# Performance work log

Hardware: AMD Instinct MI355X
Metric: run time of the kernel (lower is better)

The kernel has to match this reference:

```python
import jax, jax.numpy as jnp
import numpy as np

D_MODEL = 256
INPUT_DIM = 63
NUM_CLASSES = 13
NUM_LAYERS = 4
D_STATE = 128
D_CONV = 4
D_INNER = 512          # expand * d_model
HEADDIM = 64
NHEADS = D_INNER // HEADDIM  # 8
NGROUPS = 1
CONV_DIM = D_INNER + 2 * NGROUPS * D_STATE   # 768
D_IN_PROJ = 2 * D_INNER + 2 * NGROUPS * D_STATE + NHEADS  # 1160
BATCH, SEQLEN = 8, 2048


def setup_inputs() -> dict:
    key = jax.random.key(0)
    ks = jax.random.split(key, 12)
    s = 0.02
    f32 = jnp.float32
    # dt_bias init as in mamba2: inverse-softplus of dt in [1e-3, 1e-1]
    dt = jnp.exp(jax.random.uniform(ks[6], (NUM_LAYERS, NHEADS), f32) * (np.log(0.1) - np.log(0.001)) + np.log(0.001))
    dt_bias = dt + jnp.log(-jnp.expm1(-dt))
    A_log = jnp.log(jax.random.uniform(ks[7], (NUM_LAYERS, NHEADS), f32, 1.0, 16.0))
    return {
        "x": jax.random.normal(ks[0], (BATCH, SEQLEN, INPUT_DIM), f32),
        "in_w": jax.random.normal(ks[1], (D_MODEL, INPUT_DIM), f32) * s,
        "in_b": jnp.zeros((D_MODEL,), f32),
        "ln_in_g": jnp.ones((D_MODEL,), f32),
        "ln_in_b": jnp.zeros((D_MODEL,), f32),
        "inproj_w": jax.random.normal(ks[2], (NUM_LAYERS, D_IN_PROJ, D_MODEL), f32) * s,
        "conv_w": jax.random.normal(ks[3], (NUM_LAYERS, CONV_DIM, D_CONV), f32) * 0.2,
        "conv_b": jnp.zeros((NUM_LAYERS, CONV_DIM), f32),
        "dt_bias": dt_bias,
        "A_log": A_log,
        "D": jnp.ones((NUM_LAYERS, NHEADS), f32),
        "norm_w": jnp.ones((NUM_LAYERS, D_INNER), f32),
        "outproj_w": jax.random.normal(ks[4], (NUM_LAYERS, D_MODEL, D_INNER), f32) * s,
        "ln_g": jnp.ones((NUM_LAYERS, D_MODEL), f32),
        "ln_b": jnp.zeros((NUM_LAYERS, D_MODEL), f32),
        "out_w": jax.random.normal(ks[5], (NUM_CLASSES, D_MODEL), f32) * s,
        "out_b": jnp.zeros((NUM_CLASSES,), f32),
    }


def layernorm(x, g, b, eps=1e-5):
    m = jnp.mean(x, -1, keepdims=True)
    v = jnp.mean(jnp.square(x - m), -1, keepdims=True)
    return (x - m) * jax.lax.rsqrt(v + eps) * g + b


def mamba2_block(x, w_in, cw, cb, dtb, Alog, Dp, nw, w_out):
    # x: (b, l, d_model)
    b, l, _ = x.shape
    zxbcdt = jnp.einsum('bld,ed->ble', x, w_in)                 # (b,l,1160)
    z = zxbcdt[..., :D_INNER]                                   # (b,l,512)
    xBC = zxbcdt[..., D_INNER:D_INNER + CONV_DIM]               # (b,l,768)
    dt = jax.nn.softplus(zxbcdt[..., D_INNER + CONV_DIM:] + dtb)  # (b,l,8)
    # causal depthwise conv1d + silu
    xp = jnp.pad(xBC, ((0, 0), (D_CONV - 1, 0), (0, 0)))
    kern = cw.T[:, None, :]                                     # (K,1,C)
    xBC = jax.lax.conv_general_dilated(
        xp, kern, (1,), 'VALID',
        dimension_numbers=('NWC', 'WIO', 'NWC'),
        feature_group_count=CONV_DIM)
    xBC = jax.nn.silu(xBC + cb)
    xin = xBC[..., :D_INNER].reshape(b, l, NHEADS, HEADDIM)     # (b,l,h,p)
    Bm = xBC[..., D_INNER:D_INNER + D_STATE]                    # (b,l,n)
    Cm = xBC[..., D_INNER + D_STATE:]                           # (b,l,n)
    A = -jnp.exp(Alog)                                          # (h,)
    dA = jnp.exp(dt * A)                                        # (b,l,h)
    dtx = dt[..., None] * xin                                   # (b,l,h,p)

    def step(state, inp):
        dA_t, dtx_t, B_t, C_t = inp                             # (b,h),(b,h,p),(b,n),(b,n)
        state = state * dA_t[..., None, None] + dtx_t[..., None] * B_t[:, None, None, :]
        y_t = jnp.einsum('bhpn,bn->bhp', state, C_t)
        return state, y_t

    state0 = jnp.zeros((b, NHEADS, HEADDIM, D_STATE), x.dtype)
    _, ys = jax.lax.scan(step, state0, (
        dA.transpose(1, 0, 2), dtx.transpose(1, 0, 2, 3),
        Bm.transpose(1, 0, 2), Cm.transpose(1, 0, 2)))
    y = ys.transpose(1, 0, 2, 3) + Dp[:, None] * xin            # (b,l,h,p)
    y = y.reshape(b, l, D_INNER)
    # gated RMSNorm (norm_before_gate=False): rmsnorm(y * silu(z)) * w
    y = y * jax.nn.silu(z)
    y = y * jax.lax.rsqrt(jnp.mean(jnp.square(y), -1, keepdims=True) + 1e-5) * nw
    return jnp.einsum('ble,de->bld', y, w_out)


def reference(x, in_w, in_b, ln_in_g, ln_in_b, inproj_w, conv_w, conv_b,
              dt_bias, A_log, D, norm_w, outproj_w, ln_g, ln_b, out_w, out_b):
    # input projection (dropout is identity in eval mode)
    h = layernorm(jnp.einsum('bli,di->bld', x, in_w) + in_b, ln_in_g, ln_in_b)
    for i in range(NUM_LAYERS):
        res = h
        h = mamba2_block(h, inproj_w[i], conv_w[i], conv_b[i], dt_bias[i],
                         A_log[i], D[i], norm_w[i], outproj_w[i])
        h = layernorm(h + res, ln_g[i], ln_b[i])
    logits = jnp.einsum('bld,cd->blc', h, out_w) + out_b
    return logits.transpose(1, 0, 2)  # (T, N, C) for CTC
```

## Files before the change

### kernel.cpp

```cpp
#include <hip/hip_runtime.h>
#include <math.h>


#define NTOK   16384
#define DMODEL 256
#define DINNER 512
#define DSTATE 128
#define NHEADS 8
#define HEADDIM 64
#define CONVDIM 768
#define DINPROJ 1288
#define NPADIN 1408
#define Q      128
#define NCHUNK 16
#define NBC    128

typedef __attribute__((ext_vector_type(8))) short bf16x8v;
typedef __attribute__((ext_vector_type(4))) float f32x4;
typedef __attribute__((ext_vector_type(8))) unsigned short ush8;
typedef __attribute__((ext_vector_type(4))) unsigned short ush4;

__device__ __forceinline__ float siluf_(float x){ return x / (1.f + expf(-x)); }

__device__ __forceinline__ unsigned short f2bf(float x){
  union { float f; unsigned u; } v; v.f = x;
  unsigned r = v.u + 0x7FFF + ((v.u >> 16) & 1);
  return (unsigned short)(r >> 16);
}
__device__ __forceinline__ float bf2f(unsigned short u){
  union { unsigned u; float f; } v; v.u = ((unsigned)u) << 16; return v.f;
}
__device__ __forceinline__ void g2lds16(const void* g, void* l){
  __builtin_amdgcn_global_load_lds(
      (const __attribute__((address_space(1))) unsigned int*)g,
      (__attribute__((address_space(3))) unsigned int*)l, 16, 0, 0);
}

__global__ __launch_bounds__(256) void k_cast_all(const float* __restrict__ x,
    const float* __restrict__ in_w, const float* __restrict__ inproj_w,
    const float* __restrict__ outproj_w, unsigned short* __restrict__ xb,
    unsigned short* __restrict__ wxb, unsigned short* __restrict__ wbin,
    unsigned short* __restrict__ wbout){
  int idx = blockIdx.x*256 + threadIdx.x;
  if (idx < 1048576){
    int col = idx & 63, row = idx >> 6;
    xb[idx] = (col < 63) ? f2bf(x[(size_t)row*63 + col]) : 0;
    return;
  }
  idx -= 1048576;
  if (idx < 16384){
    int k = idx & 63, n = idx >> 6;
    wxb[idx] = (k < 63) ? f2bf(in_w[(size_t)n*63 + k]) : 0;
    return;
  }
  idx -= 16384;
  if (idx < 1441792){
    int k = idx & 255;
    int n = (idx >> 8) % NPADIN;
    int l = idx / (256*NPADIN);
    wbin[idx] = (n < DINPROJ) ? f2bf(inproj_w[((size_t)l*DINPROJ + n)*256 + k]) : 0;
    return;
  }
  idx -= 1441792;
  if (idx < 524288) wbout[idx] = f2bf(outproj_w[idx]);
}

__global__ __launch_bounds__(256) void gemm_ln(const unsigned short* __restrict__ A,
    const unsigned short* __restrict__ W, float* __restrict__ h,
    unsigned short* __restrict__ hb, const float* __restrict__ g,
    const float* __restrict__ be, int K, int addres){
  __shared__ unsigned short As[64*64];
  __shared__ unsigned short Ws[256*64];
  __shared__ float redS[4][64], redS2[4][64];
  int m0 = blockIdx.x * 64;
  int t = threadIdx.x;
  int wave = t >> 6, lane = t & 63;
  int lr = lane & 15, lk = lane >> 4;
  f32x4 acc[4][4] = {};
  for (int k0=0; k0<K; k0+=64){
    #pragma unroll
    for (int i=0;i<2;i++){
      int seg = i*256 + t;
      int row = seg >> 3, c8 = (seg&7)*8;
      g2lds16(A + (size_t)(m0+row)*K + k0 + c8, (char*)As + seg*16);
    }
    #pragma unroll
    for (int i=0;i<8;i++){
      int seg = i*256 + t;
      int row = seg >> 3, c8 = (seg&7)*8;
      g2lds16(W + (size_t)row*K + k0 + c8, (char*)Ws + seg*16);
    }
    __syncthreads();
    #pragma unroll
    for (int kk=0;kk<2;kk++){
      bf16x8v wf[4], af[4];
      #pragma unroll
      for (int ci=0;ci<4;ci++)
        wf[ci] = *(const bf16x8v*)&Ws[(wave*64 + ci*16 + lr)*64 + kk*32 + lk*8];
      #pragma unroll
      for (int ti=0;ti<4;ti++)
        af[ti] = *(const bf16x8v*)&As[(ti*16 + lr)*64 + kk*32 + lk*8];
      #pragma unroll
      for (int ci=0;ci<4;ci++)
        #pragma unroll
        for (int ti=0;ti<4;ti++)
          acc[ci][ti] = __builtin_amdgcn_mfma_f32_16x16x32_bf16(wf[ci], af[ti], acc[ci][ti],0,0,0);
    }
    __syncthreads();
  }
  float pS[4] = {}, pS2[4] = {};
  #pragma unroll
  for (int ci=0;ci<4;ci++){
    int col = wave*64 + ci*16 + lk*4;
    #pragma unroll
    for (int ti=0;ti<4;ti++){
      int token = m0 + ti*16 + lr;
      if (addres){
        float4 r4 = *(const float4*)&h[(size_t)token*256 + col];
        acc[ci][ti][0]+=r4.x; acc[ci][ti][1]+=r4.y; acc[ci][ti][2]+=r4.z; acc[ci][ti][3]+=r4.w;
      }
      #pragma unroll
      for (int j=0;j<4;j++){ float v = acc[ci][ti][j]; pS[ti]+=v; pS2[ti]+=v*v; }
    }
  }
  #pragma unroll
  for (int ti=0;ti<4;ti++){
    pS[ti]  += __shfl_xor(pS[ti],16);  pS[ti]  += __shfl_xor(pS[ti],32);
    pS2[ti] += __shfl_xor(pS2[ti],16); pS2[ti] += __shfl_xor(pS2[ti],32);
  }
  if (lk == 0){
    #pragma unroll
    for (int ti=0;ti<4;ti++){ redS[wave][ti*16+lr] = pS[ti]; redS2[wave][ti*16+lr] = pS2[ti]; }
  }
  __syncthreads();
  #pragma unroll
  for (int ti=0;ti<4;ti++){
    int rloc = ti*16 + lr;
    float S  = redS[0][rloc]+redS[1][rloc]+redS[2][rloc]+redS[3][rloc];
    float S2 = redS2[0][rloc]+redS2[1][rloc]+redS2[2][rloc]+redS2[3][rloc];
    float mean = S*(1.f/256.f);
    float var  = S2*(1.f/256.f) - mean*mean;
    float r = rsqrtf(var + 1e-5f);
    int token = m0 + rloc;
    #pragma unroll
    for (int ci=0;ci<4;ci++){
      int col = wave*64 + ci*16 + lk*4;
      float o[4];
      #pragma unroll
      for (int j=0;j<4;j++) o[j] = (acc[ci][ti][j]-mean)*r*g[col+j] + be[col+j];
      *(float4*)&h[(size_t)token*256 + col] = make_float4(o[0],o[1],o[2],o[3]);
      ush4 ub = {f2bf(o[0]),f2bf(o[1]),f2bf(o[2]),f2bf(o[3])};
      *(ush4*)&hb[(size_t)token*256 + col] = ub;
    }
  }
}

__global__ __launch_bounds__(256) void gemm_gln(
    const unsigned short* __restrict__ yssmb,
    const unsigned short* __restrict__ zxb,
    const float* __restrict__ nw, const unsigned short* __restrict__ W,
    float* __restrict__ h, unsigned short* __restrict__ hb,
    const float* __restrict__ g, const float* __restrict__ be){
  __shared__ unsigned short As[32*64];
  __shared__ unsigned short Ws[256*64];
  __shared__ float rnS[32];
  __shared__ float redS[4][32], redS2[4][32];
  int m0 = blockIdx.x * 32;
  int t = threadIdx.x;
  int wave = t >> 6, lane = t & 63;
  int lr = lane & 15, lk = lane >> 4;
  int grow = t >> 3;
  int gk   = (t & 7) * 8;
  int gtoken = m0 + grow;
  float s2 = 0.f;
  f32x4 acc[4][2] = {};
  for (int k0=0; k0<512; k0+=64){
    #pragma unroll
    for (int i=0;i<8;i++){
      int sg = i*256 + t;
      int rw = sg >> 3, c8 = (sg&7)*8;
      g2lds16(W + (size_t)rw*DINNER + k0 + c8, (char*)Ws + sg*16);
    }
    {
      int k = k0 + gk;
      ush8 ys = *(const ush8*)&yssmb[(size_t)gtoken*DINNER + k];
      ush8 z8 = *(const ush8*)&zxb[(size_t)gtoken*DINPROJ + k];
      float4 w0 = *(const float4*)&nw[k];
      float4 w1 = *(const float4*)&nw[k+4];
      float nwv[8] = {w0.x,w0.y,w0.z,w0.w,w1.x,w1.y,w1.z,w1.w};
      unsigned short vb[8];
      #pragma unroll
      for (int j=0;j<8;j++){
        float v = bf2f(ys[j]) * siluf_(bf2f(z8[j]));
        s2 += v*v;
        vb[j] = f2bf(v * nwv[j]);
      }
      *(ush8*)&As[grow*64 + gk] = *(ush8*)vb;
    }
    __syncthreads();
    #pragma unroll
    for (int kk=0;kk<2;kk++){
      bf16x8v wf[4], af[2];
      #pragma unroll
      for (int ci=0;ci<4;ci++)
        wf[ci] = *(const bf16x8v*)&Ws[(wave*64 + ci*16 + lr)*64 + kk*32 + lk*8];
      #pragma unroll
      for (int ti=0;ti<2;ti++)
        af[ti] = *(const bf16x8v*)&As[(ti*16 + lr)*64 + kk*32 + lk*8];
      #pragma unroll
      for (int ci=0;ci<4;ci++)
        #pragma unroll
        for (int ti=0;ti<2;ti++)
          acc[ci][ti] = __builtin_amdgcn_mfma_f32_16x16x32_bf16(wf[ci], af[ti], acc[ci][ti],0,0,0);
    }
    __syncthreads();
  }
  s2 += __shfl_xor(s2,1); s2 += __shfl_xor(s2,2); s2 += __shfl_xor(s2,4);
  if ((t & 7) == 0) rnS[grow] = rsqrtf(s2*(1.f/512.f) + 1e-5f);
  __syncthreads();
  float pS[2] = {}, pS2[2] = {};
  #pragma unroll
  for (int ci=0;ci<4;ci++){
    int col = wave*64 + ci*16 + lk*4;
    #pragma unroll
    for (int ti=0;ti<2;ti++){
      int tok = m0 + ti*16 + lr;
      float rn = rnS[ti*16 + lr];
      float4 r4 = *(const float4*)&h[(size_t)tok*256 + col];
      acc[ci][ti][0] = fmaf(acc[ci][ti][0], rn, r4.x);
      acc[ci][ti][1] = fmaf(acc[ci][ti][1], rn, r4.y);
      acc[ci][ti][2] = fmaf(acc[ci][ti][2], rn, r4.z);
      acc[ci][ti][3] = fmaf(acc[ci][ti][3], rn, r4.w);
      #pragma unroll
      for (int j=0;j<4;j++){ float v = acc[ci][ti][j]; pS[ti]+=v; pS2[ti]+=v*v; }
    }
  }
  #pragma unroll
  for (int ti=0;ti<2;ti++){
    pS[ti]  += __shfl_xor(pS[ti],16);  pS[ti]  += __shfl_xor(pS[ti],32);
    pS2[ti] += __shfl_xor(pS2[ti],16); pS2[ti] += __shfl_xor(pS2[ti],32);
  }
  if (lk == 0){
    #pragma unroll
    for (int ti=0;ti<2;ti++){ redS[wave][ti*16+lr] = pS[ti]; redS2[wave][ti*16+lr] = pS2[ti]; }
  }
  __syncthreads();
  #pragma unroll
  for (int ti=0;ti<2;ti++){
    int rloc = ti*16 + lr;
    float S  = redS[0][rloc]+redS[1][rloc]+redS[2][rloc]+redS[3][rloc];
    float S2 = redS2[0][rloc]+redS2[1][rloc]+redS2[2][rloc]+redS2[3][rloc];
    float mean = S*(1.f/256.f);
    float var  = S2*(1.f/256.f) - mean*mean;
    float r = rsqrtf(var + 1e-5f);
    int tok = m0 + rloc;
    #pragma unroll
    for (int ci=0;ci<4;ci++){
      int col = wave*64 + ci*16 + lk*4;
      float o[4];
      #pragma unroll
      for (int j=0;j<4;j++) o[j] = (acc[ci][ti][j]-mean)*r*g[col+j] + be[col+j];
      *(float4*)&h[(size_t)tok*256 + col] = make_float4(o[0],o[1],o[2],o[3]);
      ush4 ub = {f2bf(o[0]),f2bf(o[1]),f2bf(o[2]),f2bf(o[3])};
      *(ush4*)&hb[(size_t)tok*256 + col] = ub;
    }
  }
}

__global__ __launch_bounds__(256) void gemm_in(const unsigned short* __restrict__ A,
    const unsigned short* __restrict__ W, unsigned short* __restrict__ zxb,
    const float* __restrict__ dt_bias, const float* __restrict__ A_log,
    float* __restrict__ dtg, float* __restrict__ Lag, float* __restrict__ Tg,
    float* __restrict__ wgb){
  __shared__ unsigned short As[128*64];
  __shared__ unsigned short Ws[128*64];
  int bid = blockIdx.x;
  int wgid = (bid & 7) * 176 + (bid >> 3);
  int mtile = wgid / 11;
  int ytile = wgid % 11;
  int m0 = mtile * 128;
  int n0 = ytile * 128;
  int t = threadIdx.x;
  int wave = t >> 6, lane = t & 63;
  int wt = wave >> 1, wn = wave & 1;
  int lr = lane & 15, lk = lane >> 4;
  f32x4 acc[4][4] = {};
  for (int k0=0; k0<DMODEL; k0+=64){
    #pragma unroll
    for (int i=0;i<4;i++){
      int seg = i*256 + t;
      int row = seg >> 3, c8 = (seg&7)*8;
      g2lds16(A + (size_t)(m0+row)*DMODEL + k0 + c8, (char*)As + seg*16);
      g2lds16(W + (size_t)(n0+row)*DMODEL + k0 + c8, (char*)Ws + seg*16);
    }
    __syncthreads();
    #pragma unroll
    for (int kk=0;kk<2;kk++){
      bf16x8v wf[4], af[4];
      #pragma unroll
      for (int ci=0;ci<4;ci++)
        wf[ci] = *(const bf16x8v*)&Ws[(wn*64 + ci*16 + lr)*64 + kk*32 + lk*8];
      #pragma unroll
      for (int ti=0;ti<4;ti++)
        af[ti] = *(const bf16x8v*)&As[(wt*64 + ti*16 + lr)*64 + kk*32 + lk*8];
      #pragma unroll
      for (int ci=0;ci<4;ci++)
        #pragma unroll
        for (int ti=0;ti<4;ti++)
          acc[ci][ti] = __builtin_amdgcn_mfma_f32_16x16x32_bf16(wf[ci], af[ti], acc[ci][ti],0,0,0);
    }
    __syncthreads();
  }
  #pragma unroll
  for (int ci=0;ci<4;ci++){
    int col4 = n0 + wn*64 + ci*16 + lk*4;
    if (col4 < DINPROJ){
      #pragma unroll
      for (int ti=0;ti<4;ti++){
        int token = m0 + wt*64 + ti*16 + lr;
        ush4 ub = {f2bf(acc[ci][ti][0]),f2bf(acc[ci][ti][1]),
                   f2bf(acc[ci][ti][2]),f2bf(acc[ci][ti][3])};
        *(ush4*)&zxb[(size_t)token*DINPROJ + col4] = ub;
      }
    }
  }
  if (ytile == 10){
    float* dls = (float*)As;
    if (wn == 0 && lk < 2){
      #pragma unroll
      for (int ti=0;ti<4;ti++){
        int token = wt*64 + ti*16 + lr;
        #pragma unroll
        for (int j=0;j<4;j++) dls[token*8 + lk*4 + j] = acc[0][ti][j];
      }
    }
    __syncthreads();
    int bc = mtile;
    int rowc = m0;
    #pragma unroll
    for (int hi=0; hi<2; hi++){
      int hh = wave*2 + hi;
      float Aa = -expf(A_log[hh]);
      float bias = dt_bias[hh];
      int t0 = 2*lane, t1 = 2*lane+1;
      float r0v = dls[t0*8+hh] + bias;
      float r1v = dls[t1*8+hh] + bias;
      float d0 = (r0v > 20.f) ? r0v : log1pf(expf(r0v));
      float d1 = (r1v > 20.f) ? r1v : log1pf(expf(r1v));
      float v0 = d0*Aa, v1 = d1*Aa;
      float run = v0 + v1;
      #pragma unroll
      for (int off=1; off<64; off<<=1){
        float nb = __shfl_up(run, off);
        if (lane >= off) run += nb;
      }
      float La1 = run;
      float La0 = run - v1;
      float La_last = __shfl(run, 63);
      dtg[(size_t)(rowc+t0)*8 + hh] = d0;
      dtg[(size_t)(rowc+t1)*8 + hh] = d1;
      Lag[(size_t)(rowc+t0)*8 + hh] = La0;
      Lag[(size_t)(rowc+t1)*8 + hh] = La1;
      wgb[(size_t)(bc*8+hh)*Q + t0] = expf(La_last - La0) * d0;
      wgb[(size_t)(bc*8+hh)*Q + t1] = expf(La_last - La1) * d1;
      if (lane == 63) Tg[bc*8 + hh] = expf(La1);
    }
  }
}

__global__ __launch_bounds__(256) void k_conv(const unsigned short* __restrict__ zxb,
    const float* __restrict__ cw, const float* __restrict__ cb,
    unsigned short* __restrict__ xbcb, unsigned short* __restrict__ Xt,
    unsigned short* __restrict__ Bt){
  int tid = threadIdx.x;
  int c0 = (blockIdx.x * 8 + (tid & 7)) * 8;
  int tg = blockIdx.y * 32 + (tid >> 3);
  int r0 = tg * 8;
  int l0 = r0 & 2047;
  float kw[4][8], bias[8];
  #pragma unroll
  for (int j=0;j<8;j++){
    float4 k4 = *(const float4*)&cw[(c0+j)*4];
    kw[0][j]=k4.x; kw[1][j]=k4.y; kw[2][j]=k4.z; kw[3][j]=k4.w;
    bias[j] = cb[c0+j];
  }
  float zv[11][8];
  #pragma unroll
  for (int i=0;i<11;i++){
    if (l0 - 3 + i >= 0){
      ush8 v = *(const ush8*)&zxb[(size_t)(r0-3+i)*DINPROJ + 512 + c0];
      #pragma unroll
      for (int j=0;j<8;j++) zv[i][j] = bf2f(v[j]);
    } else {
      #pragma unroll
      for (int j=0;j<8;j++) zv[i][j] = 0.f;
    }
  }
  unsigned short ob[8][8];
  #pragma unroll
  for (int tt=0;tt<8;tt++){
    #pragma unroll
    for (int j=0;j<8;j++){
      float acc = bias[j] + zv[tt][j]*kw[0][j] + zv[tt+1][j]*kw[1][j]
                + zv[tt+2][j]*kw[2][j] + zv[tt+3][j]*kw[3][j];
      ob[tt][j] = f2bf(siluf_(acc));
    }
    *(ush8*)&xbcb[(size_t)(r0+tt)*CONVDIM + c0] = *(ush8*)ob[tt];
  }
  if (c0 < 640){
    int bc = r0 >> 7, s0 = r0 & 127;
    #pragma unroll
    for (int j=0;j<8;j++){
      ush8 col = {ob[0][j],ob[1][j],ob[2][j],ob[3][j],ob[4][j],ob[5][j],ob[6][j],ob[7][j]};
      int d = c0 + j;
      unsigned short* dst = (d < 512)
          ? (Xt + ((size_t)bc*512 + d)*Q + s0)
          : (Bt + ((size_t)bc*128 + (d-512))*Q + s0);
      *(ush8*)dst = col;
    }
  }
}

__global__ __launch_bounds__(256) void k_cbp1(const unsigned short* __restrict__ xbcb,
    const unsigned short* __restrict__ Bt, const unsigned short* __restrict__ Xt,
    const float* __restrict__ wg, unsigned short* __restrict__ CBb,
    unsigned short* __restrict__ statesB){
  __shared__ char smem[52736];
  int tid = threadIdx.x;
  int bid = blockIdx.x;
  int wgid = (bid & 7) * 144 + (bid >> 3);
  int bc = wgid / 9;
  int yy = wgid % 9;
  int wave = tid >> 6, lane = tid & 63;
  int lr = lane & 15, lk = lane >> 4;
  if (yy == 8){
    unsigned short* Cs = (unsigned short*)smem;
    unsigned short* Bs = (unsigned short*)(smem + 16384);
    int rowc = bc * Q;
    int wS = wave >> 1, wT = wave & 1;
    f32x4 acc[4][4] = {};
    for (int k0 = 0; k0 < DSTATE; k0 += 64){
      #pragma unroll
      for (int i=0;i<4;i++){
        int seg = i*256 + tid;
        int row = seg >> 3;
        int c8  = (seg & 7) * 8;
        g2lds16(xbcb + (size_t)(rowc+row)*CONVDIM + 640 + k0 + c8, Cs + seg*8);
        g2lds16(xbcb + (size_t)(rowc+row)*CONVDIM + 512 + k0 + c8, Bs + seg*8);
      }
      __syncthreads();
      #pragma unroll
      for (int kk=0; kk<2; kk++){
        bf16x8v bS[4], cT[4];
        #pragma unroll
        for (int si=0;si<4;si++)
          bS[si] = *(const bf16x8v*)&Bs[(wS*64 + si*16 + lr)*64 + kk*32 + lk*8];
        #pragma unroll
        for (int ti=0;ti<4;ti++)
          cT[ti] = *(const bf16x8v*)&Cs[(wT*64 + ti*16 + lr)*64 + kk*32 + lk*8];
        #pragma unroll
        for (int si=0;si<4;si++)
          #pragma unroll
          for (int ti=0;ti<4;ti++)
            acc[si][ti] = __builtin_amdgcn_mfma_f32_16x16x32_bf16(bS[si], cT[ti], acc[si][ti],0,0,0);
      }
      __syncthreads();
    }
    unsigned short* out = CBb + (size_t)bc * (Q*Q);
    #pragma unroll
    for (int si=0;si<4;si++){
      int s4 = wS*64 + si*16 + lk*4;
      #pragma unroll
      for (int ti=0;ti<4;ti++){
        int tt = wT*64 + ti*16 + lr;
        ush4 ub = {f2bf(acc[si][ti][0]),f2bf(acc[si][ti][1]),
                   f2bf(acc[si][ti][2]),f2bf(acc[si][ti][3])};
        *(ush4*)&out[tt*Q + s4] = ub;
      }
    }
  } else {
    int h = yy;
    int b = bc >> 4, c = bc & 15;
    unsigned short* Bw = (unsigned short*)smem;
    unsigned short* Xs = (unsigned short*)(smem + 34816);
    float* wv = (float*)(smem + 52224);
    if (tid < Q) wv[tid] = wg[(size_t)(bc*8+h)*Q + tid];
    __syncthreads();
    #pragma unroll
    for (int it=0; it<8; it++){
      int seg = it*256 + tid;
      int n = seg >> 4;
      int s8 = (seg & 15) * 8;
      ush8 u = *(const ush8*)&Bt[(size_t)bc*128*Q + n*Q + s8];
      ush8 o;
      #pragma unroll
      for (int j=0;j<8;j++) o[j] = f2bf(bf2f(u[j]) * wv[s8+j]);
      *(ush8*)&Bw[n*136 + s8] = o;
    }
    #pragma unroll
    for (int it=0; it<4; it++){
      int seg = it*256 + tid;
      int p = seg >> 4;
      int s8 = (seg & 15) * 8;
      *(ush8*)&Xs[p*136 + s8] = *(const ush8*)&Xt[(size_t)bc*512*Q + (h*64+p)*Q + s8];
    }
    __syncthreads();
    int wn = wave >> 1, wp = wave & 1;
    f32x4 acc[4][2] = {};
    #pragma unroll
    for (int ks=0; ks<4; ks++){
      bf16x8v a[4], x[2];
      #pragma unroll
      for (int mi=0;mi<4;mi++)
        a[mi] = *(const bf16x8v*)&Bw[(wn*64 + mi*16 + lr)*136 + ks*32 + lk*8];
      #pragma unroll
      for (int ni=0;ni<2;ni++)
        x[ni] = *(const bf16x8v*)&Xs[(wp*32 + ni*16 + lr)*136 + ks*32 + lk*8];
      #pragma unroll
      for (int mi=0;mi<4;mi++)
        #pragma unroll
        for (int ni=0;ni<2;ni++)
          acc[mi][ni] = __builtin_amdgcn_mfma_f32_16x16x32_bf16(a[mi], x[ni], acc[mi][ni], 0, 0, 0);
    }
    unsigned short* st = statesB + ((size_t)(b*8+h)*16 + c) * (DSTATE*HEADDIM);
    #pragma unroll
    for (int mi=0;mi<4;mi++)
      #pragma unroll
      for (int ni=0;ni<2;ni++){
        int p = wp*32 + ni*16 + lr;
        int nb = wn*64 + mi*16 + lk*4;
        ush4 ub = {f2bf(acc[mi][ni][0]),f2bf(acc[mi][ni][1]),
                   f2bf(acc[mi][ni][2]),f2bf(acc[mi][ni][3])};
        *(ush4*)&st[p*DSTATE + nb] = ub;
      }
  }
}

__global__ __launch_bounds__(256) void k_pass2(const unsigned short* __restrict__ statesB,
    const float* __restrict__ T, unsigned short* __restrict__ st0b){
  int e = blockIdx.x*256 + threadIdx.x;
  int bh = e >> 13;
  int np = e & 8191;
  int b = bh >> 3, h = bh & 7;
  size_t base = (size_t)bh * NCHUNK * 8192 + np;
  float run = 0.f;
  #pragma unroll
  for (int c=0; c<NCHUNK; c++){
    float g = bf2f(statesB[base + (size_t)c*8192]);
    st0b[base + (size_t)c*8192] = f2bf(run);
    run = fmaf(T[(b*NCHUNK+c)*8 + h], run, g);
  }
}

__global__ __launch_bounds__(256) void k_pass3(const unsigned short* __restrict__ xbcb,
    const unsigned short* __restrict__ Xt, const unsigned short* __restrict__ CBb,
    const unsigned short* __restrict__ st0b, const float* __restrict__ dt,
    const float* __restrict__ La, const float* __restrict__ Dp,
    unsigned short* __restrict__ yssmb){
  int bid = blockIdx.x;
  int wgid = (bid & 7) * 128 + (bid >> 3);
  int bc = wgid >> 3;
  int h  = wgid & 7;
  int b = bc >> 4, c = bc & 15;
  int rowc = bc * Q;
  int tid = threadIdx.x;
  __shared__ unsigned short bufA[128*136];
  __shared__ unsigned short bufB[64*136];
  __shared__ float La_s[Q], dt_s[Q], eLa_s[Q];
  if (tid < Q){
    float Lv = La[(size_t)(rowc+tid)*8 + h];
    La_s[tid] = Lv;
    dt_s[tid] = dt[(size_t)(rowc+tid)*8 + h];
    eLa_s[tid] = expf(Lv);
  }
  #pragma unroll
  for (int it=0; it<8; it++){
    int seg = it*256 + tid;
    int tt = seg >> 4;
    int n8 = (seg & 15) * 8;
    *(ush8*)&bufA[tt*136 + n8] = *(const ush8*)&xbcb[(size_t)(rowc+tt)*CONVDIM + 640 + n8];
  }
  const unsigned short* S0 = st0b + ((size_t)(b*8+h)*16 + c) * 8192;
  #pragma unroll
  for (int it=0; it<4; it++){
    int seg = it*256 + tid;
    int p = seg >> 4;
    int n8 = (seg & 15) * 8;
    *(ush8*)&bufB[p*136 + n8] = *(const ush8*)&S0[p*DSTATE + n8];
  }
  __syncthreads();
  int wave = tid >> 6, lane = tid & 63;
  int wt = wave >> 1, wp = wave & 1;
  int lr = lane & 15, lk = lane >> 4;
  f32x4 acc[2][4] = {};
  #pragma unroll
  for (int ks=0; ks<4; ks++){
    bf16x8v sf[2], cf[4];
    #pragma unroll
    for (int pi=0;pi<2;pi++)
      sf[pi] = *(const bf16x8v*)&bufB[(wp*32 + pi*16 + lr)*136 + ks*32 + lk*8];
    #pragma unroll
    for (int ti=0;ti<4;ti++)
      cf[ti] = *(const bf16x8v*)&bufA[(wt*64 + ti*16 + lr)*136 + ks*32 + lk*8];
    #pragma unroll
    for (int pi=0;pi<2;pi++)
      #pragma unroll
      for (int ti=0;ti<4;ti++)
        acc[pi][ti] = __builtin_amdgcn_mfma_f32_16x16x32_bf16(sf[pi], cf[ti], acc[pi][ti],0,0,0);
  }
  #pragma unroll
  for (int ti=0;ti<4;ti++){
    float e = eLa_s[wt*64 + ti*16 + lr];
    #pragma unroll
    for (int pi=0;pi<2;pi++)
      #pragma unroll
      for (int j=0;j<4;j++) acc[pi][ti][j] *= e;
  }
  __syncthreads();
  #pragma unroll
  for (int it=0; it<16; it++){
    int seg = it*256 + tid;
    int tt = seg >> 5;
    int s4 = (seg & 31) * 4;
    ush4 cb4 = *(const ush4*)&CBb[(size_t)bc*(Q*Q) + tt*Q + s4];
    float Lt = La_s[tt];
    ush4 m;
    #pragma unroll
    for (int j=0;j<4;j++){
      int s = s4 + j;
      float v = (s <= tt) ? bf2f(cb4[j]) * expf(Lt - La_s[s]) * dt_s[s] : 0.f;
      m[j] = f2bf(v);
    }
    *(ush4*)&bufA[tt*136 + s4] = m;
  }
  #pragma unroll
  for (int it=0; it<4; it++){
    int seg = it*256 + tid;
    int p = seg >> 4;
    int s8 = (seg & 15) * 8;
    *(ush8*)&bufB[p*136 + s8] = *(const ush8*)&Xt[(size_t)bc*512*Q + (h*64+p)*Q + s8];
  }
  __syncthreads();
  #pragma unroll
  for (int ks=0; ks<4; ks++){
    bf16x8v xf[2], mf[4];
    #pragma unroll
    for (int pi=0;pi<2;pi++)
      xf[pi] = *(const bf16x8v*)&bufB[(wp*32 + pi*16 + lr)*136 + ks*32 + lk*8];
    #pragma unroll
    for (int ti=0;ti<4;ti++)
      mf[ti] = *(const bf16x8v*)&bufA[(wt*64 + ti*16 + lr)*136 + ks*32 + lk*8];
    #pragma unroll
    for (int pi=0;pi<2;pi++)
      #pragma unroll
      for (int ti=0;ti<4;ti++)
        acc[pi][ti] = __builtin_amdgcn_mfma_f32_16x16x32_bf16(xf[pi], mf[ti], acc[pi][ti],0,0,0);
  }
  float Dh = Dp[h];
  #pragma unroll
  for (int pi=0;pi<2;pi++){
    int p4 = wp*32 + pi*16 + lk*4;
    #pragma unroll
    for (int ti=0;ti<4;ti++){
      int tt = wt*64 + ti*16 + lr;
      float o[4];
      #pragma unroll
      for (int j=0;j<4;j++)
        o[j] = fmaf(Dh, bf2f(bufB[(p4+j)*136 + tt]), acc[pi][ti][j]);
      ush4 ub = {f2bf(o[0]),f2bf(o[1]),f2bf(o[2]),f2bf(o[3])};
      *(ush4*)&yssmb[(size_t)(rowc+tt)*DINNER + h*64 + p4] = ub;
    }
  }
}

__global__ __launch_bounds__(256) void k_logits(const unsigned short* __restrict__ hb,
    const float* __restrict__ ow, const float* __restrict__ ob,
    float* __restrict__ out){
  int idx = blockIdx.x*256 + threadIdx.x;
  if (idx >= 2048*8*13) return;
  int c = idx % 13;
  int bb = (idx/13) & 7;
  int l = idx / 104;
  const ush8* hr = (const ush8*)(hb + (size_t)(bb*2048 + l)*256);
  const float4* wr = (const float4*)(ow + c*256);
  float acc = ob[c];
  #pragma unroll 4
  for (int d=0; d<32; d++){
    ush8 a = hr[d];
    float4 w0 = wr[d*2], w1 = wr[d*2+1];
    acc += bf2f(a[0])*w0.x + bf2f(a[1])*w0.y + bf2f(a[2])*w0.z + bf2f(a[3])*w0.w
         + bf2f(a[4])*w1.x + bf2f(a[5])*w1.y + bf2f(a[6])*w1.z + bf2f(a[7])*w1.w;
  }
  out[idx] = acc;
}

extern "C" void kernel_launch(void* const* d_in, const int* in_sizes, int n_in,
                              void* d_out, int out_size, void* d_ws, size_t ws_size,
                              hipStream_t stream) {
  const float* x        = (const float*)d_in[0];
  const float* in_w     = (const float*)d_in[1];
  const float* ln_in_g  = (const float*)d_in[3];
  const float* ln_in_b  = (const float*)d_in[4];
  const float* inproj_w = (const float*)d_in[5];
  const float* conv_w   = (const float*)d_in[6];
  const float* conv_b   = (const float*)d_in[7];
  const float* dt_bias  = (const float*)d_in[8];
  const float* A_log    = (const float*)d_in[9];
  const float* Dp       = (const float*)d_in[10];
  const float* norm_w   = (const float*)d_in[11];
  const float* outproj_w= (const float*)d_in[12];
  const float* ln_g     = (const float*)d_in[13];
  const float* ln_b     = (const float*)d_in[14];
  const float* out_w    = (const float*)d_in[15];
  const float* out_b    = (const float*)d_in[16];

  float* ws = (float*)d_ws;
  float* h      = ws;
  float* dtg    = ws +  4194304;
  float* Lag    = ws +  4325376;
  float* Tg     = ws +  4456448;
  float* wg     = ws +  4457472;
  unsigned short* statesB = (unsigned short*)(ws +  5506048);
  unsigned short* st0b    = (unsigned short*)(ws +  9700352);
  unsigned short* zxb     = (unsigned short*)(ws + 13894656);
  unsigned short* xbcb    = (unsigned short*)(ws + 24445952);
  unsigned short* Xt      = (unsigned short*)(ws + 30737408);
  unsigned short* Bt      = (unsigned short*)(ws + 34931712);
  unsigned short* CBb     = (unsigned short*)(ws + 35980288);
  unsigned short* yssmb   = (unsigned short*)(ws + 37028864);
  unsigned short* hb      = (unsigned short*)(ws + 41223168);
  unsigned short* xb      = (unsigned short*)(ws + 43320320);
  unsigned short* wxb     = (unsigned short*)(ws + 43844608);
  unsigned short* wbin    = (unsigned short*)(ws + 43852800);
  unsigned short* wbout   = (unsigned short*)(ws + 44573696);

  k_cast_all<<<11840, 256, 0, stream>>>(x, in_w, inproj_w, outproj_w,
      xb, wxb, wbin, wbout);
  gemm_ln<<<NTOK/64, 256, 0, stream>>>(xb, wxb, h, hb, ln_in_g, ln_in_b, 64, 0);

  for (int i=0; i<4; i++){
    gemm_in<<<1408, 256, 0, stream>>>(
        hb, wbin + (size_t)i*NPADIN*DMODEL, zxb,
        dt_bias + i*NHEADS, A_log + i*NHEADS, dtg, Lag, Tg, wg);
    k_conv<<<dim3(12, 64), 256, 0, stream>>>(zxb, conv_w + (size_t)i*CONVDIM*4,
        conv_b + i*CONVDIM, xbcb, Xt, Bt);
    k_cbp1<<<1152, 256, 0, stream>>>(xbcb, Bt, Xt, wg, CBb, statesB);
    k_pass2<<<2048, 256, 0, stream>>>(statesB, Tg, st0b);
    k_pass3<<<1024, 256, 0, stream>>>(xbcb, Xt, CBb, st0b, dtg, Lag,
        Dp + i*NHEADS, yssmb);
    gemm_gln<<<NTOK/32, 256, 0, stream>>>(yssmb, zxb,
        norm_w + i*DINNER, wbout + (size_t)i*DMODEL*DINNER,
        h, hb, ln_g + i*DMODEL, ln_b + i*DMODEL);
  }

  k_logits<<<(2048*8*13 + 255)/256, 256, 0, stream>>>(hb, out_w, out_b, (float*)d_out);
}
```

Before: 561.2 us.

## Fuse inter-chunk state scan into pass3 by recomputing prefix per block

Removes the separate k_pass2 kernel that scanned chunk states sequentially and wrote st0b. Each pass3 block now recomputes its own initial state by folding the prior chunks' states with the decay factors. This saves a kernel launch and the st0b write/read round trip, but costs redundant work, since block for chunk c rereads c prior state tiles (quadratic in chunk count, average ~7.5 tiles). The running sum also stays in fp32 across chunks instead of rounding to bf16 on store.

```diff
diff --git a/kernel.cpp b/kernel.cpp
--- a/kernel.cpp
+++ b/kernel.cpp
@@ -536,27 +536,11 @@
   }
 }
 
-__global__ __launch_bounds__(256) void k_pass2(const unsigned short* __restrict__ statesB,
-    const float* __restrict__ T, unsigned short* __restrict__ st0b){
-  int e = blockIdx.x*256 + threadIdx.x;
-  int bh = e >> 13;
-  int np = e & 8191;
-  int b = bh >> 3, h = bh & 7;
-  size_t base = (size_t)bh * NCHUNK * 8192 + np;
-  float run = 0.f;
-  #pragma unroll
-  for (int c=0; c<NCHUNK; c++){
-    float g = bf2f(statesB[base + (size_t)c*8192]);
-    st0b[base + (size_t)c*8192] = f2bf(run);
-    run = fmaf(T[(b*NCHUNK+c)*8 + h], run, g);
-  }
-}
-
 __global__ __launch_bounds__(256) void k_pass3(const unsigned short* __restrict__ xbcb,
     const unsigned short* __restrict__ Xt, const unsigned short* __restrict__ CBb,
-    const unsigned short* __restrict__ st0b, const float* __restrict__ dt,
-    const float* __restrict__ La, const float* __restrict__ Dp,
-    unsigned short* __restrict__ yssmb){
+    const unsigned short* __restrict__ statesB, const float* __restrict__ Tg,
+    const float* __restrict__ dt, const float* __restrict__ La,
+    const float* __restrict__ Dp, unsigned short* __restrict__ yssmb){
   int bid = blockIdx.x;
   int wgid = (bid & 7) * 128 + (bid >> 3);
   int bc = wgid >> 3;
@@ -580,13 +564,24 @@
     int n8 = (seg & 15) * 8;
     *(ush8*)&bufA[tt*136 + n8] = *(const ush8*)&xbcb[(size_t)(rowc+tt)*CONVDIM + 640 + n8];
   }
-  const unsigned short* S0 = st0b + ((size_t)(b*8+h)*16 + c) * 8192;
+  const unsigned short* Gbase = statesB + (size_t)(b*8+h)*16*8192;
+  const float* Tbase = Tg + b*NCHUNK*8 + h;
   #pragma unroll
   for (int it=0; it<4; it++){
     int seg = it*256 + tid;
     int p = seg >> 4;
     int n8 = (seg & 15) * 8;
-    *(ush8*)&bufB[p*136 + n8] = *(const ush8*)&S0[p*DSTATE + n8];
+    float run[8] = {0.f,0.f,0.f,0.f,0.f,0.f,0.f,0.f};
+    for (int cc=0; cc<c; cc++){
+      float Tv = Tbase[cc*8];
+      ush8 g8 = *(const ush8*)&Gbase[(size_t)cc*8192 + p*DSTATE + n8];
+      #pragma unroll
+      for (int j=0;j<8;j++) run[j] = fmaf(Tv, run[j], bf2f(g8[j]));
+    }
+    unsigned short sb[8];
+    #pragma unroll
+    for (int j=0;j<8;j++) sb[j] = f2bf(run[j]);
+    *(ush8*)&bufB[p*136 + n8] = *(ush8*)sb;
   }
   __syncthreads();
   int wave = tid >> 6, lane = tid & 63;
@@ -721,7 +716,6 @@
   float* Tg     = ws +  4456448;
   float* wg     = ws +  4457472;
   unsigned short* statesB = (unsigned short*)(ws +  5506048);
-  unsigned short* st0b    = (unsigned short*)(ws +  9700352);
   unsigned short* zxb     = (unsigned short*)(ws + 13894656);
   unsigned short* xbcb    = (unsigned short*)(ws + 24445952);
   unsigned short* Xt      = (unsigned short*)(ws + 30737408);
@@ -745,8 +739,7 @@
     k_conv<<<dim3(12, 64), 256, 0, stream>>>(zxb, conv_w + (size_t)i*CONVDIM*4,
         conv_b + i*CONVDIM, xbcb, Xt, Bt);
     k_cbp1<<<1152, 256, 0, stream>>>(xbcb, Bt, Xt, wg, CBb, statesB);
-    k_pass2<<<2048, 256, 0, stream>>>(statesB, Tg, st0b);
-    k_pass3<<<1024, 256, 0, stream>>>(xbcb, Xt, CBb, st0b, dtg, Lag,
+    k_pass3<<<1024, 256, 0, stream>>>(xbcb, Xt, CBb, statesB, Tg, dtg, Lag,
         Dp + i*NHEADS, yssmb);
     gemm_gln<<<NTOK/32, 256, 0, stream>>>(yssmb, zxb,
         norm_w + i*DINNER, wbout + (size_t)i*DMODEL*DINNER,
```

New measurement: 588.6 us. +4.9%, slower.
